# Performance work log

Hardware: AMD Instinct MI355X
Metric: run time of the kernel (lower is better)

## Reference

```python
import jax, jax.numpy as jnp
import numpy as np

N = 50000
E = 800000
IN_DIM = 256
OUT_DIM = 128
HEADS = 4
D_K = OUT_DIM // HEADS  # 32
BETA = 1.0  # beta_init, requires_grad=False (constant)
NEG_SLOPE = 0.2
EPS = 1e-12


def setup_inputs() -> dict:
    key = jax.random.key(0)
    k = jax.random.split(key, 8)
    H = jax.random.normal(k[0], (N, IN_DIM), dtype=jnp.float32)
    edge_index = jax.random.randint(k[1], (2, E), 0, N, dtype=jnp.int64)
    sim1_edge = jax.random.normal(k[2], (E,), dtype=jnp.float32)
    # Parameters (torch nn.Linear stores weight as (out, in); y = x @ W.T)
    W = jax.random.normal(k[3], (HEADS * D_K, IN_DIM), dtype=jnp.float32) * (1.0 / np.sqrt(IN_DIM))
    a_src = jax.random.normal(k[4], (HEADS, D_K), dtype=jnp.float32)
    a_dst = jax.random.normal(k[5], (HEADS, D_K), dtype=jnp.float32)
    msg_lin_w = jax.random.normal(k[6], (D_K, D_K), dtype=jnp.float32) * (1.0 / np.sqrt(D_K))
    return {"H": H, "edge_index": edge_index, "sim1_edge": sim1_edge,
            "W": W, "a_src": a_src, "a_dst": a_dst, "msg_lin_w": msg_lin_w}


def reference(H, edge_index, sim1_edge, W, a_src, a_dst, msg_lin_w):
    n = H.shape[0]
    H_proj = (H @ W.T).reshape(n, HEADS, D_K)           # [N, h, d_k]
    src, dst = edge_index[0], edge_index[1]
    h_src = H_proj[src]                                  # [E, h, d_k]
    h_dst = H_proj[dst]                                  # [E, h, d_k]
    # per-edge attention logits (struct + semantic)
    e = (jnp.einsum('ehd,hd->eh', h_src, a_src)
         + jnp.einsum('ehd,hd->eh', h_dst, a_dst)
         + BETA * sim1_edge[:, None])                    # [E, h]
    e = jnp.where(e >= 0, e, NEG_SLOPE * e)              # LeakyReLU(0.2)
    # global (per-head) max for stabilization, matching original e.max(dim=0)
    e = e - jnp.max(e, axis=0, keepdims=True)
    exp_e = jnp.exp(e)                                   # [E, h]
    denom = jax.ops.segment_sum(exp_e, dst, num_segments=n)  # [N, h]
    alpha = exp_e / (denom[dst] + EPS)                   # [E, h]  (dropout p=0 -> identity)
    m = alpha[:, :, None] * h_src                        # [E, h, d_k]
    out = jax.ops.segment_sum(m, dst, num_segments=n)    # [N, h, d_k]
    out_h = out.reshape(n, HEADS * D_K)                  # concat=True
    msg_base = jnp.einsum('ehd,od->eho', h_src, msg_lin_w).mean(axis=1)  # [E, d_k]
    alpha_mean = alpha.mean(axis=1)                      # [E]
    return out_h, alpha_mean, msg_base
```

## Files before the change

### kernel.cpp

```cpp
#include <hip/hip_runtime.h>
#include <hip/hip_bf16.h>
#include <hip/hip_fp16.h>
#include <float.h>

#define HEADS 4
#define DK 32

static constexpr float kBeta = 1.0f;
static constexpr float kNeg  = 0.2f;
static constexpr float kEps  = 1e-12f;

typedef __bf16 bf16x8 __attribute__((ext_vector_type(8)));
typedef float  f32x4  __attribute__((ext_vector_type(4)));

__device__ __forceinline__ float bf2f(unsigned short v) {
  return __uint_as_float((unsigned)v << 16);
}
__device__ __forceinline__ unsigned short f2bf(float f) {
  unsigned u = __float_as_uint(f);
  unsigned r = u + 0x7FFFu + ((u >> 16) & 1u);
  return (unsigned short)(r >> 16);
}
__device__ __forceinline__ unsigned fkey(float x) {
  unsigned u = __float_as_uint(x);
  return (u & 0x80000000u) ? ~u : (u | 0x80000000u);
}
__device__ __forceinline__ float funkey(unsigned k) {
  unsigned u = (k & 0x80000000u) ? (k & 0x7fffffffu) : ~k;
  return __uint_as_float(u);
}
__device__ __forceinline__ bf16x8 as8(uint4 v) {
  union { uint4 u; bf16x8 b; } x; x.u = v; return x.b;
}

__global__ __launch_bounds__(256) void k_detect(const int* __restrict__ ei32,
                                                const unsigned* __restrict__ Hw,
                                                int* __restrict__ eflag,
                                                int* __restrict__ dflag,
                                                int E, int nw) {
  int i = blockIdx.x * 256 + threadIdx.x;
  if (i < 4096 && 2 * i + 1 < 2 * E && ei32[2 * i + 1] != 0) atomicOr(eflag, 1);
  if (i < nw && ((Hw[i] >> 7) & 0xFFu) == 0xFFu) atomicOr(dflag, 1);
}

__global__ __launch_bounds__(256) void k_cvt(const int* __restrict__ ei32,
                                             const int* __restrict__ eflag,
                                             int* __restrict__ src_i,
                                             int* __restrict__ dst_i,
                                             int* __restrict__ deg, int E) {
  int i = blockIdx.x * 256 + threadIdx.x;
  if (i >= E) return;
  int s, d;
  if (*eflag) { s = ei32[i];     d = ei32[E + i]; }
  else        { s = ei32[2 * i]; d = ei32[2 * E + 2 * i]; }
  src_i[i] = s;
  dst_i[i] = d;
  atomicAdd(deg + d, 1);
}

__global__ __launch_bounds__(256) void k_wparams(const void* __restrict__ in,
                                                 unsigned short* __restrict__ Bhi,
                                                 unsigned short* __restrict__ Blo,
                                                 const void* __restrict__ a_src,
                                                 const void* __restrict__ a_dst,
                                                 const void* __restrict__ msg_w,
                                                 float* __restrict__ af,
                                                 float* __restrict__ msgwf,
                                                 const int* __restrict__ dflag) {
  const int dt = *dflag;
  if (blockIdx.x < 128) {
    int i = blockIdx.x * 256 + threadIdx.x;
    int r = i >> 8, c = i & 255;
    float v = dt ? ((const float*)in)[i] : bf2f(((const unsigned short*)in)[i]);
    unsigned short hb = f2bf(v);
    unsigned short lb = f2bf(v - bf2f(hb));
    int kt = c >> 5, ct = r >> 4;
    int lane = (((c >> 3) & 3) << 4) | (r & 15);
    int idx = ((kt * 8 + ct) * 64 + lane) * 8 + (c & 7);
    Bhi[idx] = hb;
    Blo[idx] = lb;
  } else {
    int i = (blockIdx.x - 128) * 256 + threadIdx.x;
    if (i < 128) {
      af[i] = dt ? ((const float*)a_src)[i] : bf2f(((const unsigned short*)a_src)[i]);
    } else if (i < 256) {
      int j = i - 128;
      af[i] = dt ? ((const float*)a_dst)[j] : bf2f(((const unsigned short*)a_dst)[j]);
    } else if (i < 1280) {
      int j = i - 256;
      msgwf[j] = dt ? ((const float*)msg_w)[j] : bf2f(((const unsigned short*)msg_w)[j]);
    }
  }
}

__global__ __launch_bounds__(256) void k_scan1(const int* __restrict__ deg,
                                               int* __restrict__ bsum, int N) {
  const int t = threadIdx.x;
  int i = blockIdx.x * 256 + t;
  int v = (i < N) ? deg[i] : 0;
#pragma unroll
  for (int off = 32; off; off >>= 1) v += __shfl_xor(v, off);
  __shared__ int red[4];
  if ((t & 63) == 0) red[t >> 6] = v;
  __syncthreads();
  if (t == 0) bsum[blockIdx.x] = red[0] + red[1] + red[2] + red[3];
}
__global__ __launch_bounds__(1024) void k_scan2(int* __restrict__ bsum, int nb) {
  __shared__ int part[1024];
  const int t = threadIdx.x;
  part[t] = (t < nb) ? bsum[t] : 0;
  __syncthreads();
  int own = part[t];
  for (int off = 1; off < 1024; off <<= 1) {
    int v = (t >= off) ? part[t - off] : 0;
    __syncthreads();
    part[t] += v;
    __syncthreads();
  }
  if (t < nb) bsum[t] = part[t] - own;
}
__global__ __launch_bounds__(256) void k_scan3(const int* __restrict__ deg,
                                               const int* __restrict__ bsum,
                                               int* __restrict__ row_ptr,
                                               int* __restrict__ cursor, int N) {
  __shared__ int part[256];
  const int t = threadIdx.x;
  int i = blockIdx.x * 256 + t;
  int v = (i < N) ? deg[i] : 0;
  part[t] = v;
  __syncthreads();
  for (int off = 1; off < 256; off <<= 1) {
    int x = (t >= off) ? part[t - off] : 0;
    __syncthreads();
    part[t] += x;
    __syncthreads();
  }
  int excl = part[t] - v + bsum[blockIdx.x];
  if (i < N) {
    row_ptr[i] = excl;
    cursor[i]  = excl;
    if (i == N - 1) row_ptr[N] = excl + v;
  }
}

__global__ __launch_bounds__(256) void k_proj(const void* __restrict__ Hraw,
                                              const unsigned short* __restrict__ Bhi,
                                              const unsigned short* __restrict__ Blo,
                                              const int* __restrict__ dflag,
                                              const float* __restrict__ af,
                                              const float* __restrict__ msgwf,
                                              float* __restrict__ s_src,
                                              float* __restrict__ s_dst,
                                              __half* __restrict__ msgb,
                                              __half* __restrict__ Hb, int N) {
  __shared__ uint4 lds4[4096];
  float* ldsF = (float*)lds4;
  const int t = threadIdx.x;
  const int nb = blockIdx.x * 64;
  const int dt = *dflag;
  if (dt) {
    const float4* __restrict__ H4 = (const float4*)Hraw;
#pragma unroll
    for (int it = 0; it < 8; ++it) {
      int c = it * 256 + t;
      int row = c >> 5, k8 = c & 31;
      int gr = nb + row;
      float4 v0 = make_float4(0.f, 0.f, 0.f, 0.f), v1 = v0;
      if (gr < N) {
        v0 = H4[(size_t)gr * 64 + k8 * 2];
        v1 = H4[(size_t)gr * 64 + k8 * 2 + 1];
      }
      float f[8] = {v0.x, v0.y, v0.z, v0.w, v1.x, v1.y, v1.z, v1.w};
      unsigned hi[8], lo[8];
#pragma unroll
      for (int j = 0; j < 8; ++j) {
        unsigned short hb = f2bf(f[j]);
        hi[j] = hb;
        lo[j] = f2bf(f[j] - bf2f(hb));
      }
      int slot = (k8 * 64 + row) ^ (k8 & 7);
      lds4[slot] = make_uint4(hi[0] | (hi[1] << 16), hi[2] | (hi[3] << 16),
                              hi[4] | (hi[5] << 16), hi[6] | (hi[7] << 16));
      lds4[2048 + slot] = make_uint4(lo[0] | (lo[1] << 16), lo[2] | (lo[3] << 16),
                                     lo[4] | (lo[5] << 16), lo[6] | (lo[7] << 16));
    }
  } else {
    const uint4* __restrict__ H8 = (const uint4*)Hraw;
#pragma unroll
    for (int it = 0; it < 8; ++it) {
      int c = it * 256 + t;
      int row = c >> 5, k8 = c & 31;
      int gr = nb + row;
      uint4 v = make_uint4(0u, 0u, 0u, 0u);
      if (gr < N) v = H8[(size_t)gr * 32 + k8];
      lds4[(k8 * 64 + row) ^ (k8 & 7)] = v;
    }
  }
  __syncthreads();

  const int l = t & 63;
  const int wrow = (t >> 6) * 16;
  f32x4 acc[8];
#pragma unroll
  for (int ct = 0; ct < 8; ++ct) acc[ct] = (f32x4){0.f, 0.f, 0.f, 0.f};
  const uint4* __restrict__ Bh4 = (const uint4*)Bhi;
  const uint4* __restrict__ Bl4 = (const uint4*)Blo;
  if (dt) {
#pragma unroll 2
    for (int kt = 0; kt < 8; ++kt) {
      int k8 = kt * 4 + (l >> 4);
      int slot = (k8 * 64 + wrow + (l & 15)) ^ (k8 & 7);
      bf16x8 ah = as8(lds4[slot]);
      bf16x8 al = as8(lds4[2048 + slot]);
#pragma unroll
      for (int ct = 0; ct < 8; ++ct) {
        bf16x8 bh = as8(Bh4[(kt * 8 + ct) * 64 + l]);
        bf16x8 bl = as8(Bl4[(kt * 8 + ct) * 64 + l]);
        acc[ct] = __builtin_amdgcn_mfma_f32_16x16x32_bf16(ah, bh, acc[ct], 0, 0, 0);
        acc[ct] = __builtin_amdgcn_mfma_f32_16x16x32_bf16(ah, bl, acc[ct], 0, 0, 0);
        acc[ct] = __builtin_amdgcn_mfma_f32_16x16x32_bf16(al, bh, acc[ct], 0, 0, 0);
      }
    }
  } else {
#pragma unroll 2
    for (int kt = 0; kt < 8; ++kt) {
      int k8 = kt * 4 + (l >> 4);
      int slot = (k8 * 64 + wrow + (l & 15)) ^ (k8 & 7);
      bf16x8 ah = as8(lds4[slot]);
#pragma unroll
      for (int ct = 0; ct < 8; ++ct) {
        bf16x8 bh = as8(Bh4[(kt * 8 + ct) * 64 + l]);
        acc[ct] = __builtin_amdgcn_mfma_f32_16x16x32_bf16(ah, bh, acc[ct], 0, 0, 0);
      }
    }
  }
  __syncthreads();
#pragma unroll
  for (int ct = 0; ct < 8; ++ct)
#pragma unroll
    for (int r = 0; r < 4; ++r)
      ldsF[(wrow + (l >> 4) * 4 + r) * 132 + ct * 16 + (l & 15)] = acc[ct][r];
  __syncthreads();
  for (int i = 0; i < 16; ++i) {
    int row = wrow + i, n = nb + row;
    if (n >= N) break;
    float h0 = ldsF[row * 132 + l], h1 = ldsF[row * 132 + 64 + l];
    Hb[(size_t)n * 128 + l]      = __float2half(h0);
    Hb[(size_t)n * 128 + 64 + l] = __float2half(h1);
    float p0 = h0 * af[l],       p1 = h1 * af[64 + l];
    float q0 = h0 * af[128 + l], q1 = h1 * af[192 + l];
#pragma unroll
    for (int off = 16; off; off >>= 1) {
      p0 += __shfl_xor(p0, off);
      p1 += __shfl_xor(p1, off);
      q0 += __shfl_xor(q0, off);
      q1 += __shfl_xor(q1, off);
    }
    if (l == 0)  { s_src[n*4+0] = p0; s_src[n*4+2] = p1; s_dst[n*4+0] = q0; s_dst[n*4+2] = q1; }
    if (l == 32) { s_src[n*4+1] = p0; s_src[n*4+3] = p1; s_dst[n*4+1] = q0; s_dst[n*4+3] = q1; }
    float t4 = h0 + __shfl_xor(h0, 32) + h1 + __shfl_xor(h1, 32);
    float hbar = 0.25f * t4;
    if (l < DK) {
      float acc2 = 0.f;
#pragma unroll
      for (int d = 0; d < DK; ++d) acc2 += __shfl(hbar, d) * msgwf[l * DK + d];
      msgb[(size_t)n * DK + l] = __float2half(acc2);
    }
  }
}

__global__ __launch_bounds__(256) void k_fillog(const int* __restrict__ src,
                                                const int* __restrict__ dstv,
                                                const void* __restrict__ sim1,
                                                const int* __restrict__ dflag,
                                                const float* __restrict__ s_src,
                                                const float* __restrict__ s_dst,
                                                int* __restrict__ cursor,
                                                int2* __restrict__ pack,
                                                unsigned* __restrict__ gmax, int E) {
  const int e = blockIdx.x * 256 + threadIdx.x;
  float m0 = -FLT_MAX, m1 = -FLT_MAX, m2 = -FLT_MAX, m3 = -FLT_MAX;
  if (e < E) {
    int s = src[e], d = dstv[e];
    float sv = (*dflag) ? ((const float*)sim1)[e] : bf2f(((const unsigned short*)sim1)[e]);
    int pos = atomicAdd(cursor + d, 1);
    pack[pos] = make_int2(s, __float_as_int(sv));
    float4 ss = *(const float4*)(s_src + (size_t)s * 4);
    float4 sd = *(const float4*)(s_dst + (size_t)d * 4);
    float b = kBeta * sv;
    float e0 = ss.x + sd.x + b; e0 = (e0 >= 0.f) ? e0 : kNeg * e0;
    float e1 = ss.y + sd.y + b; e1 = (e1 >= 0.f) ? e1 : kNeg * e1;
    float e2 = ss.z + sd.z + b; e2 = (e2 >= 0.f) ? e2 : kNeg * e2;
    float e3 = ss.w + sd.w + b; e3 = (e3 >= 0.f) ? e3 : kNeg * e3;
    m0 = e0; m1 = e1; m2 = e2; m3 = e3;
  }
#pragma unroll
  for (int off = 32; off; off >>= 1) {
    m0 = fmaxf(m0, __shfl_xor(m0, off));
    m1 = fmaxf(m1, __shfl_xor(m1, off));
    m2 = fmaxf(m2, __shfl_xor(m2, off));
    m3 = fmaxf(m3, __shfl_xor(m3, off));
  }
  __shared__ float red[4][4];
  if ((threadIdx.x & 63) == 0) {
    int w = threadIdx.x >> 6;
    red[w][0] = m0; red[w][1] = m1; red[w][2] = m2; red[w][3] = m3;
  }
  __syncthreads();
  if (threadIdx.x < 4) {
    int h = threadIdx.x;
    float mm = fmaxf(fmaxf(red[0][h], red[1][h]), fmaxf(red[2][h], red[3][h]));
    atomicMax(gmax + h, fkey(mm));
  }
}

__global__ __launch_bounds__(256) void k_out(const int* __restrict__ row_ptr,
                                             const int2* __restrict__ pack,
                                             const float* __restrict__ s_src,
                                             const float* __restrict__ s_dst,
                                             const unsigned* __restrict__ gmax,
                                             const unsigned* __restrict__ Hb_u,
                                             const int* __restrict__ dflag,
                                             float* __restrict__ denom,
                                             void* __restrict__ d_out, int N) {
  const int n = (int)((blockIdx.x * 256 + threadIdx.x) >> 6);
  const int l = threadIdx.x & 63;
  if (n >= N) return;
  const int beg = row_ptr[n];
  const int deg = row_ptr[n + 1] - beg;
  const int dt = *dflag;
  const float m0 = funkey(gmax[0]), m1 = funkey(gmax[1]);
  const float m2 = funkey(gmax[2]), m3 = funkey(gmax[3]);
  const float4 sd = *(const float4*)(s_dst + (size_t)n * 4);
  float accx = 0.f, accy = 0.f;
  float4 dn = make_float4(0.f, 0.f, 0.f, 0.f);
  int s = 0;
  float4 ev = make_float4(0.f, 0.f, 0.f, 0.f);
  const bool small = (deg <= 64);
  if (small) {
    if (l < deg) {
      int2 p = pack[beg + l];
      s = p.x;
      float sv = __int_as_float(p.y);
      float4 ss = *(const float4*)(s_src + (size_t)s * 4);
      float e0 = ss.x + sd.x + sv; e0 = (e0 >= 0.f) ? e0 : kNeg * e0;
      float e1 = ss.y + sd.y + sv; e1 = (e1 >= 0.f) ? e1 : kNeg * e1;
      float e2 = ss.z + sd.z + sv; e2 = (e2 >= 0.f) ? e2 : kNeg * e2;
      float e3 = ss.w + sd.w + sv; e3 = (e3 >= 0.f) ? e3 : kNeg * e3;
      ev = make_float4(expf(e0 - m0), expf(e1 - m1), expf(e2 - m2), expf(e3 - m3));
      dn = ev;
    }
  } else {
    for (int base = 0; base < deg; base += 64) {
      if (base + l < deg) {
        int2 p = pack[beg + base + l];
        float sv = __int_as_float(p.y);
        float4 ss = *(const float4*)(s_src + (size_t)p.x * 4);
        float e0 = ss.x + sd.x + sv; e0 = (e0 >= 0.f) ? e0 : kNeg * e0;
        float e1 = ss.y + sd.y + sv; e1 = (e1 >= 0.f) ? e1 : kNeg * e1;
        float e2 = ss.z + sd.z + sv; e2 = (e2 >= 0.f) ? e2 : kNeg * e2;
        float e3 = ss.w + sd.w + sv; e3 = (e3 >= 0.f) ? e3 : kNeg * e3;
        dn.x += expf(e0 - m0); dn.y += expf(e1 - m1);
        dn.z += expf(e2 - m2); dn.w += expf(e3 - m3);
      }
    }
  }
#pragma unroll
  for (int off = 32; off; off >>= 1) {
    dn.x += __shfl_xor(dn.x, off);
    dn.y += __shfl_xor(dn.y, off);
    dn.z += __shfl_xor(dn.z, off);
    dn.w += __shfl_xor(dn.w, off);
  }
  if (l == 0) *(float4*)(denom + (size_t)n * 4) = make_float4(dn.x, dn.y, dn.z, dn.w);
  const float i0 = 1.f / (dn.x + kEps), i1 = 1.f / (dn.y + kEps);
  const float i2 = 1.f / (dn.z + kEps), i3 = 1.f / (dn.w + kEps);
  const float myinv = (l < 32) ? ((l < 16) ? i0 : i1) : ((l < 48) ? i2 : i3);
  if (small) {
    for (int i = 0; i < deg; ++i) {
      int si = __shfl(s, i);
      float ax = __shfl(ev.x, i), ay = __shfl(ev.y, i);
      float az = __shfl(ev.z, i), aw = __shfl(ev.w, i);
      float aa = ((l < 32) ? ((l < 16) ? ax : ay) : ((l < 48) ? az : aw)) * myinv;
      unsigned u = Hb_u[(size_t)si * 64 + l];
      float2 f = __half22float2(*(const __half2*)&u);
      accx += aa * f.x;
      accy += aa * f.y;
    }
  } else {
    for (int base = 0; base < deg; base += 64) {
      int cnt = min(64, deg - base);
      int s2 = 0;
      float4 e2v = make_float4(0.f, 0.f, 0.f, 0.f);
      if (l < cnt) {
        int2 p = pack[beg + base + l];
        s2 = p.x;
        float sv = __int_as_float(p.y);
        float4 ss = *(const float4*)(s_src + (size_t)s2 * 4);
        float e0 = ss.x + sd.x + sv; e0 = (e0 >= 0.f) ? e0 : kNeg * e0;
        float e1 = ss.y + sd.y + sv; e1 = (e1 >= 0.f) ? e1 : kNeg * e1;
        float e2 = ss.z + sd.z + sv; e2 = (e2 >= 0.f) ? e2 : kNeg * e2;
        float e3 = ss.w + sd.w + sv; e3 = (e3 >= 0.f) ? e3 : kNeg * e3;
        e2v = make_float4(expf(e0 - m0), expf(e1 - m1), expf(e2 - m2), expf(e3 - m3));
      }
      for (int i = 0; i < cnt; ++i) {
        int si = __shfl(s2, i);
        float ax = __shfl(e2v.x, i), ay = __shfl(e2v.y, i);
        float az = __shfl(e2v.z, i), aw = __shfl(e2v.w, i);
        float aa = ((l < 32) ? ((l < 16) ? ax : ay) : ((l < 48) ? az : aw)) * myinv;
        unsigned u = Hb_u[(size_t)si * 64 + l];
        float2 f = __half22float2(*(const __half2*)&u);
        accx += aa * f.x;
        accy += aa * f.y;
      }
    }
  }
  if (dt) {
    *(float2*)&((float*)d_out)[(size_t)n * 128 + 2 * l] = make_float2(accx, accy);
  } else {
    __hip_bfloat162 b = __float22bfloat162_rn(make_float2(accx, accy));
    *(__hip_bfloat162*)((__hip_bfloat16*)d_out + (size_t)n * 128 + 2 * l) = b;
  }
}

__global__ __launch_bounds__(256) void k_edge(const int* __restrict__ src,
                                              const int* __restrict__ dstv,
                                              const void* __restrict__ sim1,
                                              const int* __restrict__ dflag,
                                              const float* __restrict__ s_src,
                                              const float* __restrict__ s_dst,
                                              const float* __restrict__ denom,
                                              const unsigned* __restrict__ gmax,
                                              const __half2* __restrict__ msgb2,
                                              void* __restrict__ d_out,
                                              int N, int E) {
  long long tid = (long long)blockIdx.x * 256 + threadIdx.x;
  if (tid >= (long long)E * 16) return;
  int e = (int)(tid >> 4), jp = (int)(tid & 15);
  const int dt = *dflag;
  int s = src[e];
  __half2 hv = msgb2[(size_t)s * 16 + jp];
  float2 f = __half22float2(hv);
  const size_t alpha_off = (size_t)N * 128;
  const size_t msg_off = alpha_off + (size_t)E;
  if (dt) {
    *(float2*)&((float*)d_out)[msg_off + (size_t)e * 32 + 2 * jp] = f;
  } else {
    __hip_bfloat162 b = __float22bfloat162_rn(f);
    *(__hip_bfloat162*)((__hip_bfloat16*)d_out + msg_off + (size_t)e * 32 + 2 * jp) = b;
  }
  if (jp == 0) {
    int d = dstv[e];
    float sv = dt ? ((const float*)sim1)[e] : bf2f(((const unsigned short*)sim1)[e]);
    float4 ss = *(const float4*)(s_src + (size_t)s * 4);
    float4 sd = *(const float4*)(s_dst + (size_t)d * 4);
    float4 dn = *(const float4*)(denom + (size_t)d * 4);
    float m0 = funkey(gmax[0]), m1 = funkey(gmax[1]);
    float m2 = funkey(gmax[2]), m3 = funkey(gmax[3]);
    float b = kBeta * sv;
    float e0 = ss.x + sd.x + b; e0 = (e0 >= 0.f) ? e0 : kNeg * e0;
    float e1 = ss.y + sd.y + b; e1 = (e1 >= 0.f) ? e1 : kNeg * e1;
    float e2 = ss.z + sd.z + b; e2 = (e2 >= 0.f) ? e2 : kNeg * e2;
    float e3 = ss.w + sd.w + b; e3 = (e3 >= 0.f) ? e3 : kNeg * e3;
    float am = 0.25f * (expf(e0 - m0) / (dn.x + kEps) + expf(e1 - m1) / (dn.y + kEps) +
                        expf(e2 - m2) / (dn.z + kEps) + expf(e3 - m3) / (dn.w + kEps));
    if (dt) ((float*)d_out)[alpha_off + e] = am;
    else    ((__hip_bfloat16*)d_out)[alpha_off + e] = __float2bfloat16(am);
  }
}

extern "C" void kernel_launch(void* const* d_in, const int* in_sizes, int n_in,
                              void* d_out, int out_size, void* d_ws, size_t ws_size,
                              hipStream_t stream) {
  const void* H     = d_in[0];
  const int*  ei    = (const int*)d_in[1];
  const void* sim1  = d_in[2];
  const void* W     = d_in[3];
  const void* a_src = d_in[4];
  const void* a_dst = d_in[5];
  const void* msg_w = d_in[6];
  const int N = in_sizes[0] / 256;
  const int E = in_sizes[2];
  const int NB = (N + 255) / 256;

  char* base     = (char*)d_ws;
  float* s_src   = (float*)base;  base += (size_t)N * 4 * 4;
  float* s_dst   = (float*)base;  base += (size_t)N * 4 * 4;
  __half* msgb   = (__half*)base; base += (size_t)N * DK * 2;
  __half* Hb     = (__half*)base; base += (size_t)N * 128 * 2;
  float* denom   = (float*)base;  base += (size_t)N * 4 * 4;
  unsigned short* Bhi = (unsigned short*)base; base += 32768 * 2;
  unsigned short* Blo = (unsigned short*)base; base += 32768 * 2;
  int* deg       = (int*)base;    base += (size_t)N * 4;
  unsigned* gmax = (unsigned*)base; base += 4 * 4;
  int* eflag     = (int*)base;    base += 4;
  int* dflag     = (int*)base;    base += 4;
  int* row_ptr   = (int*)base;    base += (size_t)(N + 2) * 4;
  int* cursor    = (int*)base;    base += (size_t)N * 4;
  int* bsum      = (int*)base;    base += 1024 * 4;
  int2* pack     = (int2*)base;   base += (size_t)E * 8;
  int* src_i     = (int*)base;    base += (size_t)E * 4;
  int* dst_i     = (int*)base;    base += (size_t)E * 4;
  float* af      = (float*)base;  base += 256 * 4;
  float* msgwf   = (float*)base;  base += 1024 * 4;

  hipMemsetAsync(deg, 0, (size_t)(N + 6) * sizeof(int), stream);

  k_detect<<<512, 256, 0, stream>>>(ei, (const unsigned*)H, eflag, dflag, E, 131072);
  k_cvt<<<(E + 255) / 256, 256, 0, stream>>>(ei, eflag, src_i, dst_i, deg, E);
  k_wparams<<<133, 256, 0, stream>>>(W, Bhi, Blo, a_src, a_dst, msg_w, af, msgwf, dflag);
  k_proj<<<(N + 63) / 64, 256, 0, stream>>>(H, Bhi, Blo, dflag, af, msgwf,
                                            s_src, s_dst, msgb, Hb, N);
  k_scan1<<<NB, 256, 0, stream>>>(deg, bsum, N);
  k_scan2<<<1, 1024, 0, stream>>>(bsum, NB);
  k_scan3<<<NB, 256, 0, stream>>>(deg, bsum, row_ptr, cursor, N);
  k_fillog<<<(E + 255) / 256, 256, 0, stream>>>(src_i, dst_i, sim1, dflag, s_src, s_dst,
                                                cursor, pack, gmax, E);
  k_out<<<(int)(((size_t)N * 64 + 255) / 256), 256, 0, stream>>>(
      row_ptr, pack, s_src, s_dst, gmax, (const unsigned*)Hb, dflag, denom, d_out, N);
  k_edge<<<(int)(((long long)E * 16 + 255) / 256), 256, 0, stream>>>(
      src_i, dst_i, sim1, dflag, s_src, s_dst, denom, gmax, (const __half2*)msgb,
      d_out, N, E);
}
```

Before: 477.7 us.

## Halve k_proj LDS, split hi/lo passes, compute epilogue from MFMA registers

The projection kernel's LDS tile shrinks from 64KB to 32KB by staging only the bf16 hi part first and then reloading H to build the lo residual in a second pass, which should allow more blocks per CU. The epilogue no longer writes the full fp32 tile to LDS and loops row by row. Attention scores are reduced with shuffles straight from the MFMA accumulators, and the message projection uses an LDS-staged weight and per-wave mean buffer. The cost is reading H from global memory twice in fp32 mode, plus scattered 2-byte Hb stores that are less coalesced.

```diff
diff --git a/kernel.cpp b/kernel.cpp
--- a/kernel.cpp
+++ b/kernel.cpp
@@ -153,11 +153,23 @@
                                               float* __restrict__ s_dst,
                                               __half* __restrict__ msgb,
                                               __half* __restrict__ Hb, int N) {
-  __shared__ uint4 lds4[4096];
+  __shared__ uint4 lds4[2048];
   float* ldsF = (float*)lds4;
   const int t = threadIdx.x;
   const int nb = blockIdx.x * 64;
   const int dt = *dflag;
+  const int l = t & 63;
+  const int wv = t >> 6;
+  const int wrow = wv * 16;
+  const int c16 = l & 15;
+  const int g4 = l >> 4;
+
+  f32x4 acc[8];
+#pragma unroll
+  for (int ct = 0; ct < 8; ++ct) acc[ct] = (f32x4){0.f, 0.f, 0.f, 0.f};
+  const uint4* __restrict__ Bh4 = (const uint4*)Bhi;
+  const uint4* __restrict__ Bl4 = (const uint4*)Blo;
+
   if (dt) {
     const float4* __restrict__ H4 = (const float4*)Hraw;
 #pragma unroll
@@ -171,18 +183,12 @@
         v1 = H4[(size_t)gr * 64 + k8 * 2 + 1];
       }
       float f[8] = {v0.x, v0.y, v0.z, v0.w, v1.x, v1.y, v1.z, v1.w};
-      unsigned hi[8], lo[8];
-#pragma unroll
-      for (int j = 0; j < 8; ++j) {
-        unsigned short hb = f2bf(f[j]);
-        hi[j] = hb;
-        lo[j] = f2bf(f[j] - bf2f(hb));
-      }
-      int slot = (k8 * 64 + row) ^ (k8 & 7);
-      lds4[slot] = make_uint4(hi[0] | (hi[1] << 16), hi[2] | (hi[3] << 16),
-                              hi[4] | (hi[5] << 16), hi[6] | (hi[7] << 16));
-      lds4[2048 + slot] = make_uint4(lo[0] | (lo[1] << 16), lo[2] | (lo[3] << 16),
-                                     lo[4] | (lo[5] << 16), lo[6] | (lo[7] << 16));
+      unsigned hi[8];
+#pragma unroll
+      for (int j = 0; j < 8; ++j) hi[j] = f2bf(f[j]);
+      lds4[(k8 * 64 + row) ^ (k8 & 7)] =
+          make_uint4(hi[0] | (hi[1] << 16), hi[2] | (hi[3] << 16),
+                     hi[4] | (hi[5] << 16), hi[6] | (hi[7] << 16));
     }
   } else {
     const uint4* __restrict__ H8 = (const uint4*)Hraw;
@@ -197,74 +203,145 @@
     }
   }
   __syncthreads();
-
-  const int l = t & 63;
-  const int wrow = (t >> 6) * 16;
-  f32x4 acc[8];
-#pragma unroll
-  for (int ct = 0; ct < 8; ++ct) acc[ct] = (f32x4){0.f, 0.f, 0.f, 0.f};
-  const uint4* __restrict__ Bh4 = (const uint4*)Bhi;
-  const uint4* __restrict__ Bl4 = (const uint4*)Blo;
+#pragma unroll 2
+  for (int kt = 0; kt < 8; ++kt) {
+    int k8 = kt * 4 + g4;
+    int slot = (k8 * 64 + wrow + c16) ^ (k8 & 7);
+    bf16x8 ah = as8(lds4[slot]);
+#pragma unroll
+    for (int ct = 0; ct < 8; ++ct) {
+      bf16x8 bh = as8(Bh4[(kt * 8 + ct) * 64 + l]);
+      acc[ct] = __builtin_amdgcn_mfma_f32_16x16x32_bf16(ah, bh, acc[ct], 0, 0, 0);
+    }
+    if (dt) {
+#pragma unroll
+      for (int ct = 0; ct < 8; ++ct) {
+        bf16x8 bl = as8(Bl4[(kt * 8 + ct) * 64 + l]);
+        acc[ct] = __builtin_amdgcn_mfma_f32_16x16x32_bf16(ah, bl, acc[ct], 0, 0, 0);
+      }
+    }
+  }
   if (dt) {
+    __syncthreads();
+    const float4* __restrict__ H4 = (const float4*)Hraw;
+#pragma unroll
+    for (int it = 0; it < 8; ++it) {
+      int c = it * 256 + t;
+      int row = c >> 5, k8 = c & 31;
+      int gr = nb + row;
+      float4 v0 = make_float4(0.f, 0.f, 0.f, 0.f), v1 = v0;
+      if (gr < N) {
+        v0 = H4[(size_t)gr * 64 + k8 * 2];
+        v1 = H4[(size_t)gr * 64 + k8 * 2 + 1];
+      }
+      float f[8] = {v0.x, v0.y, v0.z, v0.w, v1.x, v1.y, v1.z, v1.w};
+      unsigned lo[8];
+#pragma unroll
+      for (int j = 0; j < 8; ++j) lo[j] = f2bf(f[j] - bf2f(f2bf(f[j])));
+      lds4[(k8 * 64 + row) ^ (k8 & 7)] =
+          make_uint4(lo[0] | (lo[1] << 16), lo[2] | (lo[3] << 16),
+                     lo[4] | (lo[5] << 16), lo[6] | (lo[7] << 16));
+    }
+    __syncthreads();
 #pragma unroll 2
     for (int kt = 0; kt < 8; ++kt) {
-      int k8 = kt * 4 + (l >> 4);
-      int slot = (k8 * 64 + wrow + (l & 15)) ^ (k8 & 7);
-      bf16x8 ah = as8(lds4[slot]);
-      bf16x8 al = as8(lds4[2048 + slot]);
+      int k8 = kt * 4 + g4;
+      int slot = (k8 * 64 + wrow + c16) ^ (k8 & 7);
+      bf16x8 al = as8(lds4[slot]);
 #pragma unroll
       for (int ct = 0; ct < 8; ++ct) {
         bf16x8 bh = as8(Bh4[(kt * 8 + ct) * 64 + l]);
-        bf16x8 bl = as8(Bl4[(kt * 8 + ct) * 64 + l]);
-        acc[ct] = __builtin_amdgcn_mfma_f32_16x16x32_bf16(ah, bh, acc[ct], 0, 0, 0);
-        acc[ct] = __builtin_amdgcn_mfma_f32_16x16x32_bf16(ah, bl, acc[ct], 0, 0, 0);
         acc[ct] = __builtin_amdgcn_mfma_f32_16x16x32_bf16(al, bh, acc[ct], 0, 0, 0);
       }
     }
-  } else {
-#pragma unroll 2
-    for (int kt = 0; kt < 8; ++kt) {
-      int k8 = kt * 4 + (l >> 4);
-      int slot = (k8 * 64 + wrow + (l & 15)) ^ (k8 & 7);
-      bf16x8 ah = as8(lds4[slot]);
-#pragma unroll
-      for (int ct = 0; ct < 8; ++ct) {
-        bf16x8 bh = as8(Bh4[(kt * 8 + ct) * 64 + l]);
-        acc[ct] = __builtin_amdgcn_mfma_f32_16x16x32_bf16(ah, bh, acc[ct], 0, 0, 0);
-      }
-    }
   }
   __syncthreads();
-#pragma unroll
-  for (int ct = 0; ct < 8; ++ct)
-#pragma unroll
-    for (int r = 0; r < 4; ++r)
-      ldsF[(wrow + (l >> 4) * 4 + r) * 132 + ct * 16 + (l & 15)] = acc[ct][r];
+
+#pragma unroll
+  for (int i = 0; i < 4; ++i) {
+    int idx = t * 4 + i;
+    ldsF[(idx >> 5) * 33 + (idx & 31)] = msgwf[idx];
+  }
+  float* hbuf = ldsF + 1056 + wv * 528;
+#pragma unroll
+  for (int r = 0; r < 4; ++r) {
+    float h0 = 0.25f * (acc[0][r] + acc[2][r] + acc[4][r] + acc[6][r]);
+    float h1 = 0.25f * (acc[1][r] + acc[3][r] + acc[5][r] + acc[7][r]);
+    hbuf[(g4 * 4 + r) * 33 + c16]      = h0;
+    hbuf[(g4 * 4 + r) * 33 + 16 + c16] = h1;
+  }
   __syncthreads();
-  for (int i = 0; i < 16; ++i) {
-    int row = wrow + i, n = nb + row;
-    if (n >= N) break;
-    float h0 = ldsF[row * 132 + l], h1 = ldsF[row * 132 + 64 + l];
-    Hb[(size_t)n * 128 + l]      = __float2half(h0);
-    Hb[(size_t)n * 128 + 64 + l] = __float2half(h1);
-    float p0 = h0 * af[l],       p1 = h1 * af[64 + l];
-    float q0 = h0 * af[128 + l], q1 = h1 * af[192 + l];
-#pragma unroll
-    for (int off = 16; off; off >>= 1) {
-      p0 += __shfl_xor(p0, off);
-      p1 += __shfl_xor(p1, off);
-      q0 += __shfl_xor(q0, off);
-      q1 += __shfl_xor(q1, off);
-    }
-    if (l == 0)  { s_src[n*4+0] = p0; s_src[n*4+2] = p1; s_dst[n*4+0] = q0; s_dst[n*4+2] = q1; }
-    if (l == 32) { s_src[n*4+1] = p0; s_src[n*4+3] = p1; s_dst[n*4+1] = q0; s_dst[n*4+3] = q1; }
-    float t4 = h0 + __shfl_xor(h0, 32) + h1 + __shfl_xor(h1, 32);
-    float hbar = 0.25f * t4;
-    if (l < DK) {
-      float acc2 = 0.f;
-#pragma unroll
-      for (int d = 0; d < DK; ++d) acc2 += __shfl(hbar, d) * msgwf[l * DK + d];
-      msgb[(size_t)n * DK + l] = __float2half(acc2);
+
+  float afp[8], afq[8];
+#pragma unroll
+  for (int ct = 0; ct < 8; ++ct) {
+    afp[ct] = af[ct * 16 + c16];
+    afq[ct] = af[128 + ct * 16 + c16];
+  }
+  float pv0[4], pv1[4], pv2[4], pv3[4], qv0[4], qv1[4], qv2[4], qv3[4];
+#pragma unroll
+  for (int r = 0; r < 4; ++r) {
+    pv0[r] = acc[0][r] * afp[0] + acc[1][r] * afp[1];
+    pv1[r] = acc[2][r] * afp[2] + acc[3][r] * afp[3];
+    pv2[r] = acc[4][r] * afp[4] + acc[5][r] * afp[5];
+    pv3[r] = acc[6][r] * afp[6] + acc[7][r] * afp[7];
+    qv0[r] = acc[0][r] * afq[0] + acc[1][r] * afq[1];
+    qv1[r] = acc[2][r] * afq[2] + acc[3][r] * afq[3];
+    qv2[r] = acc[4][r] * afq[4] + acc[5][r] * afq[5];
+    qv3[r] = acc[6][r] * afq[6] + acc[7][r] * afq[7];
+  }
+#pragma unroll
+  for (int off = 1; off <= 8; off <<= 1) {
+#pragma unroll
+    for (int r = 0; r < 4; ++r) {
+      pv0[r] += __shfl_xor(pv0[r], off);
+      pv1[r] += __shfl_xor(pv1[r], off);
+      pv2[r] += __shfl_xor(pv2[r], off);
+      pv3[r] += __shfl_xor(pv3[r], off);
+      qv0[r] += __shfl_xor(qv0[r], off);
+      qv1[r] += __shfl_xor(qv1[r], off);
+      qv2[r] += __shfl_xor(qv2[r], off);
+      qv3[r] += __shfl_xor(qv3[r], off);
+    }
+  }
+#pragma unroll
+  for (int r = 0; r < 4; ++r) {
+    int n = nb + wrow + g4 * 4 + r;
+    if (n < N) {
+      if (c16 < 4) {
+        float v = (c16 == 0) ? pv0[r] : (c16 == 1) ? pv1[r]
+                 : (c16 == 2) ? pv2[r] : pv3[r];
+        s_src[(size_t)n * 4 + c16] = v;
+      } else if (c16 < 8) {
+        int hh = c16 - 4;
+        float v = (hh == 0) ? qv0[r] : (hh == 1) ? qv1[r]
+                 : (hh == 2) ? qv2[r] : qv3[r];
+        s_dst[(size_t)n * 4 + hh] = v;
+      }
+    }
+  }
+#pragma unroll
+  for (int ct = 0; ct < 8; ++ct) {
+#pragma unroll
+    for (int r = 0; r < 4; ++r) {
+      int n = nb + wrow + g4 * 4 + r;
+      if (n < N) Hb[(size_t)n * 128 + ct * 16 + c16] = __float2half(acc[ct][r]);
+    }
+  }
+  {
+    const int j = l & 31;
+    const int r0 = (l >> 5) * 8;
+    float res[8] = {0.f, 0.f, 0.f, 0.f, 0.f, 0.f, 0.f, 0.f};
+#pragma unroll 4
+    for (int d = 0; d < 32; ++d) {
+      float mw = ldsF[j * 33 + d];
+#pragma unroll
+      for (int i = 0; i < 8; ++i) res[i] += hbuf[(r0 + i) * 33 + d] * mw;
+    }
+#pragma unroll
+    for (int i = 0; i < 8; ++i) {
+      int n = nb + wrow + r0 + i;
+      if (n < N) msgb[(size_t)n * 32 + j] = __float2half(res[i]);
     }
   }
 }
```

After: 465.8 us. 2.5% less time.
